# Performance work log

Hardware: AMD Instinct MI355X
Metric: run time of the kernel (lower is better)

## Reference

```python
import jax, jax.numpy as jnp
import numpy as np

B, L, DIN, H, E, K = 64, 256, 768, 64, 8, 2
S = 16  # sqrt(L): token<->feature grid side
LOSS_COEF = 1e-2


def gelu(x):
    return jax.nn.gelu(x, approximate=False)  # torch nn.GELU (exact erf)


def cv_squared(v):
    v = v.astype(jnp.float32)
    return jnp.var(v, ddof=1) / (jnp.mean(v) ** 2 + 1e-10)


def setup_inputs() -> dict:
    key = jax.random.key(0)
    ks = jax.random.split(key, 16)
    rn = lambda k, shape, s=0.02: jax.random.normal(k, shape, jnp.float32) * s
    lap = jnp.array([[0., 1., 0.], [1., -4., 1.], [0., 1., 0.]], jnp.float32)
    return {
        "x": jax.random.normal(ks[0], (B, L, DIN), jnp.float32),
        "dte": jax.random.normal(ks[1], (B, L, DIN), jnp.float32),
        "w_gate": rn(ks[2], (L, E), 1.0),
        "W_exp": rn(ks[3], (E, DIN, H)), "b_exp": jnp.zeros((E, H), jnp.float32),
        "W_sh": rn(ks[4], (DIN, H)), "b_sh": jnp.zeros((H,), jnp.float32),
        "ln_g": jnp.ones((H,), jnp.float32), "ln_b": jnp.zeros((H,), jnp.float32),
        "W_px": rn(ks[5], (H, 2 * H)), "b_px": jnp.zeros((2 * H,), jnp.float32),
        "conv_sh": jnp.tile(lap[None, None], (H, 1, 1, 1)),  # depthwise Laplacian [H,1,3,3]
        "W_pxx": rn(ks[6], (H, H)), "b_pxx": jnp.zeros((H,), jnp.float32),
        "W_dte": rn(ks[7], (H, H)), "b_dte": jnp.zeros((H,), jnp.float32),
        "W_dteall": rn(ks[8], (H, H)), "b_dteall": jnp.zeros((H,), jnp.float32),
        "W_rgb": rn(ks[9], (DIN, H)), "b_rgb": jnp.zeros((H,), jnp.float32),
        "W_fx": rn(ks[10], (H, H)), "b_fx": jnp.zeros((H,), jnp.float32),
        "W_fmod": rn(ks[11], (H, H)), "b_fmod": jnp.zeros((H,), jnp.float32),
        "W_fxx": rn(ks[12], (H, H)), "b_fxx": jnp.zeros((H,), jnp.float32),
    }


def reference(x, dte, w_gate, W_exp, b_exp, W_sh, b_sh, ln_g, ln_b, W_px, b_px,
              conv_sh, W_pxx, b_pxx, W_dte, b_dte, W_dteall, b_dteall,
              W_rgb, b_rgb, W_fx, b_fx, W_fmod, b_fmod, W_fxx, b_fxx):
    # ---- top-k gating (clean logits; noisy_gating=False / eval) ----
    logits = dte.mean(-1) @ w_gate                     # [B,E]
    topv, topi = jax.lax.top_k(logits, K)
    topg = jax.nn.softmax(topv, axis=1)
    gates = jnp.zeros_like(logits).at[jnp.arange(B)[:, None], topi].set(topg)
    importance = gates.sum(0)
    load = (gates > 0).sum(0).astype(jnp.float32)
    loss = LOSS_COEF * (cv_squared(importance) + cv_squared(load))
    # ---- sparse dispatch / expert Linear / weighted combine (dense-equivalent) ----
    y = jnp.einsum('be,bld,edh->blh', gates, dte, W_exp) + (gates @ b_exp)[:, None, :]
    # ---- shared expert Linear + Shared block ----
    sh = dte @ W_sh + b_sh                             # [B,L,H]
    shortcut = sh
    t = (sh - sh.mean(-1, keepdims=True)) * jax.lax.rsqrt(sh.var(-1, keepdims=True) + 1e-6)
    t = t * ln_g + ln_b
    t = t @ W_px + b_px                                # [B,L,2H]
    t1, t2 = t[..., :H], t[..., H:]
    f = t1.transpose(0, 2, 1).reshape(B, H, S, S)      # token2feature
    f = jax.lax.conv_general_dilated(f, conv_sh, (1, 1), 'SAME', feature_group_count=H)
    t1 = f.reshape(B, H, L).transpose(0, 2, 1)         # feature2token
    sh = (gelu(t1) * t2) @ W_pxx + b_pxx + shortcut
    # ---- combine MoE and shared streams ----
    dte_tok = (y @ W_dte + b_dte) + (sh @ W_dteall + b_dteall)
    rgb_tok = x @ W_rgb + b_rgb
    # ---- Fusion (its self.norm was overwritten to GELU; token<->feature round-trip is identity) ----
    shortcut = rgb_tok
    a = gelu(rgb_tok) @ W_fx + b_fx
    m = gelu(dte_tok) @ W_fmod + b_fmod
    out = (gelu(m) * a) @ W_fxx + b_fxx + shortcut     # [B,L,H]
    return out, loss
```

## Files before the change

### kernel.cpp

```cpp
#include <hip/hip_runtime.h>
#include <math.h>

typedef unsigned short u16;
typedef unsigned int u32;
typedef __attribute__((ext_vector_type(8))) short bf16x8;
typedef __attribute__((ext_vector_type(4))) float f32x4;


__device__ __forceinline__ float bf2f(u16 u) {
    union { u32 i; float f; } x; x.i = ((u32)u) << 16; return x.f;
}
__device__ __forceinline__ u16 f2bf(float f) {
    union { float f; u32 i; } x; x.f = f;
    u32 i = x.i;
    return (u16)((i + 0x7fffu + ((i >> 16) & 1u)) >> 16);
}
__device__ __forceinline__ u32 pack2(float a, float b) {
    return (u32)f2bf(a) | ((u32)f2bf(b) << 16);
}
__device__ __forceinline__ float wsum(float v) {
    #pragma unroll
    for (int o = 1; o < 64; o <<= 1) v += __shfl_xor(v, o, 64);
    return v;
}
__device__ __forceinline__ float gelu_f(float x) {
    return 0.5f * x * (1.0f + erff(x * 0.70710678118654752440f));
}

__global__ __launch_bounds__(256) void k_gate_part(const float* __restrict__ dte,
                                                   const float* __restrict__ w_gate,
                                                   float* __restrict__ partial) {
    __shared__ float dmeanS[64];
    int p = blockIdx.x, tid = threadIdx.x, w = tid >> 6, lane = tid & 63;
    for (int i = 0; i < 16; i++) {
        int l = w * 16 + i;
        const float* pr = dte + ((size_t)p * 64 + l) * 768;
        float s = 0.f;
        #pragma unroll
        for (int j = 0; j < 3; j++) {
            float4 v = *(const float4*)(pr + (lane + j * 64) * 4);
            s += v.x + v.y + v.z + v.w;
        }
        s = wsum(s);
        if (lane == 0) dmeanS[l] = s * (1.f / 768.f);
    }
    __syncthreads();
    if (w == 0) {
        float dm = dmeanS[lane];
        int wl = (p & 3) * 64 + lane;
        #pragma unroll
        for (int e = 0; e < 8; e++) {
            float s = wsum(dm * w_gate[wl * 8 + e]);
            if (lane == 0) partial[p * 8 + e] = s;
        }
    }
}

__global__ __launch_bounds__(256) void k_gate_fin(const float* __restrict__ partial,
                                                  const float* __restrict__ b_exp,
                                                  int* __restrict__ topi,
                                                  float* __restrict__ topg,
                                                  float* __restrict__ bias_y,
                                                  float* __restrict__ loss_out) {
    __shared__ float gS[64 * 8];
    __shared__ int i0S[64], i1S[64];
    __shared__ float g0S[64], g1S[64];
    int tid = threadIdx.x;
    if (tid < 64) {
        float lg[8];
        #pragma unroll
        for (int e = 0; e < 8; e++)
            lg[e] = partial[(tid * 4 + 0) * 8 + e] + partial[(tid * 4 + 1) * 8 + e] +
                    partial[(tid * 4 + 2) * 8 + e] + partial[(tid * 4 + 3) * 8 + e];
        int i0 = 0; float v0 = lg[0];
        #pragma unroll
        for (int e = 1; e < 8; e++) if (lg[e] > v0) { v0 = lg[e]; i0 = e; }
        int i1 = -1; float v1 = -1e30f;
        #pragma unroll
        for (int e = 0; e < 8; e++) if (e != i0 && lg[e] > v1) { v1 = lg[e]; i1 = e; }
        if (i1 < 0) i1 = (i0 + 1) & 7;
        float e2 = expf(v1 - v0);
        float g0 = 1.f / (1.f + e2);
        float g1 = e2 / (1.f + e2);
        #pragma unroll
        for (int e = 0; e < 8; e++) gS[tid * 8 + e] = 0.f;
        gS[tid * 8 + i0] = g0;
        gS[tid * 8 + i1] = g1;
        i0S[tid] = i0; i1S[tid] = i1; g0S[tid] = g0; g1S[tid] = g1;
        topi[tid * 2] = i0; topi[tid * 2 + 1] = i1;
        topg[tid * 2] = g0; topg[tid * 2 + 1] = g1;
    }
    __syncthreads();
    for (int idx = tid; idx < 4096; idx += 256) {
        int b = idx >> 6, h = idx & 63;
        bias_y[idx] = g0S[b] * b_exp[i0S[b] * 64 + h] + g1S[b] * b_exp[i1S[b] * 64 + h];
    }
    if (tid < 64) {
        float g[8];
        #pragma unroll
        for (int e = 0; e < 8; e++) g[e] = gS[tid * 8 + e];
        float imp[8], ld[8];
        #pragma unroll
        for (int e = 0; e < 8; e++) {
            imp[e] = wsum(g[e]);
            ld[e]  = wsum(g[e] > 0.f ? 1.f : 0.f);
        }
        if (tid == 0) {
            float l = 0.f;
            {
                float s = 0.f;
                #pragma unroll
                for (int e = 0; e < 8; e++) s += imp[e];
                float mn = s / 8.f, v = 0.f;
                #pragma unroll
                for (int e = 0; e < 8; e++) { float d = imp[e] - mn; v += d * d; }
                l += (v / 7.f) / (mn * mn + 1e-10f);
            }
            {
                float s = 0.f;
                #pragma unroll
                for (int e = 0; e < 8; e++) s += ld[e];
                float mn = s / 8.f, v = 0.f;
                #pragma unroll
                for (int e = 0; e < 8; e++) { float d = ld[e] - mn; v += d * d; }
                l += (v / 7.f) / (mn * mn + 1e-10f);
            }
            loss_out[0] = 0.01f * l;
        }
    }
}

__global__ __launch_bounds__(256) void k_gemm3(const float* __restrict__ dte,
                                               const float* __restrict__ x,
                                               const float* __restrict__ W_sh,
                                               const float* __restrict__ b_sh,
                                               const float* __restrict__ W_exp,
                                               const int* __restrict__ topi,
                                               const float* __restrict__ topg,
                                               const float* __restrict__ bias_y,
                                               const float* __restrict__ W_rgb,
                                               const float* __restrict__ b_rgb,
                                               float* __restrict__ buf_sh,
                                               u16* __restrict__ buf_y,
                                               float* __restrict__ out_rgb) {
    __shared__ u16 As[64 * 72];
    __shared__ u16 Wt[64 * 72];
    int bid = blockIdx.x;
    int kind, row0;
    if (bid < 512) { kind = bid & 1; row0 = (bid >> 1) * 64; }
    else           { kind = 2;       row0 = (bid - 512) * 64; }
    int b = row0 >> 8;
    int tid = threadIdx.x, wv = tid >> 6, lane = tid & 63;
    int m = lane & 15, quad = lane >> 4;

    const float* A = (kind == 2) ? x : dte;
    const float* W0 = (kind == 2) ? W_rgb : W_sh;
    const float* W1 = W0;
    float g0 = 0.f, g1 = 0.f;
    if (kind == 1) {
        W0 = W_exp + (size_t)topi[2 * b] * 49152;
        W1 = W_exp + (size_t)topi[2 * b + 1] * 49152;
        g0 = topg[2 * b]; g1 = topg[2 * b + 1];
    }

    float4 pa[2][2];
    float  pw[16];
    const int a_r  = tid >> 3;
    const int a_k8 = (tid & 7) * 8;
    const int w_n  = tid & 63;
    const int w_k0 = (tid >> 6) * 16;

    auto loadA = [&](int kc) {
        #pragma unroll
        for (int j = 0; j < 2; j++) {
            const float* src = A + (size_t)(row0 + a_r + j * 32) * 768 + kc * 64 + a_k8;
            pa[j][0] = *(const float4*)(src);
            pa[j][1] = *(const float4*)(src + 4);
        }
    };
    auto loadW = [&](int kc) {
        if (kind == 1) {
            #pragma unroll
            for (int j = 0; j < 16; j++) {
                size_t off = (size_t)(kc * 64 + w_k0 + j) * 64 + w_n;
                pw[j] = g0 * W0[off] + g1 * W1[off];
            }
        } else {
            #pragma unroll
            for (int j = 0; j < 16; j++)
                pw[j] = W0[(size_t)(kc * 64 + w_k0 + j) * 64 + w_n];
        }
    };
    auto stageLDS = [&]() {
        #pragma unroll
        for (int j = 0; j < 2; j++) {
            uint4 d;
            d.x = pack2(pa[j][0].x, pa[j][0].y);
            d.y = pack2(pa[j][0].z, pa[j][0].w);
            d.z = pack2(pa[j][1].x, pa[j][1].y);
            d.w = pack2(pa[j][1].z, pa[j][1].w);
            *(uint4*)&As[(a_r + j * 32) * 72 + a_k8] = d;
        }
        uint4 d0, d1;
        d0.x = pack2(pw[0],  pw[1]);  d0.y = pack2(pw[2],  pw[3]);
        d0.z = pack2(pw[4],  pw[5]);  d0.w = pack2(pw[6],  pw[7]);
        d1.x = pack2(pw[8],  pw[9]);  d1.y = pack2(pw[10], pw[11]);
        d1.z = pack2(pw[12], pw[13]); d1.w = pack2(pw[14], pw[15]);
        *(uint4*)&Wt[w_n * 72 + w_k0]     = d0;
        *(uint4*)&Wt[w_n * 72 + w_k0 + 8] = d1;
    };

    f32x4 acc0 = {0.f, 0.f, 0.f, 0.f}, acc1 = acc0, acc2 = acc0, acc3 = acc0;

    loadA(0); loadW(0);
    for (int kc = 0; kc < 12; kc++) {
        __syncthreads();
        stageLDS();
        __syncthreads();
        if (kc < 11) { loadA(kc + 1); loadW(kc + 1); }
        const int ar = (wv * 16 + m) * 72;
        bf16x8 a0 = *(const bf16x8*)&As[ar + quad * 8];
        bf16x8 a1 = *(const bf16x8*)&As[ar + 32 + quad * 8];
        #pragma unroll
        for (int t = 0; t < 4; t++) {
            const int br = (t * 16 + m) * 72;
            bf16x8 b0 = *(const bf16x8*)&Wt[br + quad * 8];
            bf16x8 b1 = *(const bf16x8*)&Wt[br + 32 + quad * 8];
            f32x4* accp = (t == 0) ? &acc0 : (t == 1) ? &acc1 : (t == 2) ? &acc2 : &acc3;
            *accp = __builtin_amdgcn_mfma_f32_16x16x32_bf16(a0, b0, *accp, 0, 0, 0);
            *accp = __builtin_amdgcn_mfma_f32_16x16x32_bf16(a1, b1, *accp, 0, 0, 0);
        }
    }

    f32x4 accs[4] = {acc0, acc1, acc2, acc3};
    #pragma unroll
    for (int t = 0; t < 4; t++) {
        int col = t * 16 + m;
        float bias;
        if (kind == 0)      bias = b_sh[col];
        else if (kind == 1) bias = bias_y[b * 64 + col];
        else                bias = b_rgb[col];
        #pragma unroll
        for (int i = 0; i < 4; i++) {
            int r = row0 + wv * 16 + quad * 4 + i;
            float val = accs[t][i] + bias;
            if (kind == 0)      buf_sh[(size_t)r * 64 + col] = val;
            else if (kind == 1) buf_y[(size_t)r * 64 + col] = f2bf(val);
            else                out_rgb[(size_t)r * 64 + col] = val;
        }
    }
}

__global__ __launch_bounds__(256) void k_lnpx(const float* __restrict__ buf_sh,
                                              const float* __restrict__ ln_g,
                                              const float* __restrict__ ln_b,
                                              const float* __restrict__ W_px,
                                              const float* __restrict__ b_px,
                                              u16* __restrict__ t1, u16* __restrict__ t2) {
    __shared__ float T[16 * 68];
    __shared__ float Wpx[8192];
    int r0 = blockIdx.x * 16;
    int tid = threadIdx.x, w = tid >> 6, lane = tid & 63;
    #pragma unroll
    for (int j = 0; j < 8; j++) {
        int e4 = tid + j * 256;
        *(float4*)(Wpx + e4 * 4) = *(const float4*)(W_px + e4 * 4);
    }
    float lnG = ln_g[lane], lnB = ln_b[lane];
    #pragma unroll
    for (int i = 0; i < 4; i++) {
        int l = w * 4 + i;
        float v = buf_sh[(size_t)(r0 + l) * 64 + lane];
        float mean = wsum(v) * (1.f / 64.f);
        float d = v - mean;
        float var = wsum(d * d) * (1.f / 64.f);
        T[l * 68 + lane] = d * rsqrtf(var + 1e-6f) * lnG + lnB;
    }
    __syncthreads();
    int rg = tid >> 4, cg = tid & 15;
    float acc1[4] = {}, acc2[4] = {};
    const float* tr = T + rg * 68;
    #pragma unroll 4
    for (int kk = 0; kk < 64; kk++) {
        float a0 = tr[kk];
        float4 w1 = *(const float4*)(Wpx + kk * 128 + cg * 4);
        float4 w2 = *(const float4*)(Wpx + kk * 128 + 64 + cg * 4);
        acc1[0] += a0 * w1.x; acc1[1] += a0 * w1.y; acc1[2] += a0 * w1.z; acc1[3] += a0 * w1.w;
        acc2[0] += a0 * w2.x; acc2[1] += a0 * w2.y; acc2[2] += a0 * w2.z; acc2[3] += a0 * w2.w;
    }
    float4 b1 = *(const float4*)(b_px + cg * 4);
    float4 b2 = *(const float4*)(b_px + 64 + cg * 4);
    {
        int r = r0 + rg;
        u32* d1 = (u32*)(t1 + (size_t)r * 64 + cg * 4);
        d1[0] = pack2(acc1[0] + b1.x, acc1[1] + b1.y);
        d1[1] = pack2(acc1[2] + b1.z, acc1[3] + b1.w);
        u32* d2 = (u32*)(t2 + (size_t)r * 64 + cg * 4);
        d2[0] = pack2(acc2[0] + b2.x, acc2[1] + b2.y);
        d2[1] = pack2(acc2[2] + b2.z, acc2[3] + b2.w);
    }
}

__global__ __launch_bounds__(256) void k_tail(const u16* __restrict__ t1,
                                              const u16* __restrict__ t2,
                                              const float* __restrict__ conv_sh,
                                              const float* __restrict__ W_pxx,
                                              const float* __restrict__ b_pxx,
                                              const float* __restrict__ buf_sh,
                                              const u16* __restrict__ buf_y,
                                              const float* __restrict__ W_dte,
                                              const float* __restrict__ b_dte,
                                              const float* __restrict__ W_dteall,
                                              const float* __restrict__ b_dteall,
                                              const float* __restrict__ W_fx,
                                              const float* __restrict__ b_fx,
                                              const float* __restrict__ W_fmod,
                                              const float* __restrict__ b_fmod,
                                              const float* __restrict__ W_fxx,
                                              const float* __restrict__ b_fxx,
                                              float* __restrict__ out) {
    __shared__ float C0[16 * 68];
    __shared__ float Yb[16 * 68];
    __shared__ float GA[16 * 68];
    __shared__ float SH1[16 * 68];
    __shared__ float GM[16 * 68];
    __shared__ float RS[16 * 64];
    int r0 = blockIdx.x * 16;
    int tid = threadIdx.x, w = tid >> 6, lane = tid & 63;
    int rg = tid >> 4, cg = tid & 15;

    {
        int l = tid >> 4, c = (tid & 15) * 4;
        uint2 v = *(const uint2*)(buf_y + (size_t)(r0 + l) * 64 + c);
        Yb[l * 68 + c + 0] = bf2f((u16)(v.x & 0xffffu));
        Yb[l * 68 + c + 1] = bf2f((u16)(v.x >> 16));
        Yb[l * 68 + c + 2] = bf2f((u16)(v.y & 0xffffu));
        Yb[l * 68 + c + 3] = bf2f((u16)(v.y >> 16));
    }
    {
        int l = tid >> 4, c4 = tid & 15;
        float4 rv = *(const float4*)(out + (size_t)(r0 + l) * 64 + c4 * 4);
        *(float4*)(RS + l * 64 + c4 * 4) = rv;
        GA[l * 68 + c4 * 4 + 0] = gelu_f(rv.x);
        GA[l * 68 + c4 * 4 + 1] = gelu_f(rv.y);
        GA[l * 68 + c4 * 4 + 2] = gelu_f(rv.z);
        GA[l * 68 + c4 * 4 + 3] = gelu_f(rv.w);
    }
    {
        float c0 = conv_sh[lane * 9 + 0], c1 = conv_sh[lane * 9 + 1], c2 = conv_sh[lane * 9 + 2];
        float c3 = conv_sh[lane * 9 + 3], c4 = conv_sh[lane * 9 + 4], c5 = conv_sh[lane * 9 + 5];
        float c6 = conv_sh[lane * 9 + 6], c7 = conv_sh[lane * 9 + 7], c8 = conv_sh[lane * 9 + 8];
        #pragma unroll
        for (int i = 0; i < 4; i++) {
            int l = w * 4 + i;
            int gr = r0 + l;
            int pix = gr & 255, ii = pix >> 4, jj = pix & 15;
            const u16* p = t1 + (size_t)gr * 64 + lane;
            float c = c4 * bf2f(p[0]);
            if (ii > 0) {
                c += c1 * bf2f(p[-1024]);
                if (jj > 0)  c += c0 * bf2f(p[-1024 - 64]);
                if (jj < 15) c += c2 * bf2f(p[-1024 + 64]);
            }
            if (jj > 0)  c += c3 * bf2f(p[-64]);
            if (jj < 15) c += c5 * bf2f(p[64]);
            if (ii < 15) {
                c += c7 * bf2f(p[1024]);
                if (jj > 0)  c += c6 * bf2f(p[1024 - 64]);
                if (jj < 15) c += c8 * bf2f(p[1024 + 64]);
            }
            C0[l * 68 + lane] = gelu_f(c) * bf2f(t2[(size_t)gr * 64 + lane]);
        }
    }
    __syncthreads();

    {
        float acc[4] = {};
        const float* ur = C0 + rg * 68;
        #pragma unroll 8
        for (int kk = 0; kk < 64; kk++) {
            float a0 = ur[kk];
            float4 wvv = *(const float4*)(W_pxx + kk * 64 + cg * 4);
            acc[0] += a0 * wvv.x; acc[1] += a0 * wvv.y; acc[2] += a0 * wvv.z; acc[3] += a0 * wvv.w;
        }
        float4 bp = *(const float4*)(b_pxx + cg * 4);
        float4 shv = *(const float4*)(buf_sh + (size_t)(r0 + rg) * 64 + cg * 4);
        *(float4*)(SH1 + rg * 68 + cg * 4) =
            make_float4(acc[0] + bp.x + shv.x, acc[1] + bp.y + shv.y,
                        acc[2] + bp.z + shv.z, acc[3] + bp.w + shv.w);
    }
    __syncthreads();

    {
        float acc[4] = {};
        const float* yr = Yb + rg * 68;
        const float* sr = SH1 + rg * 68;
        #pragma unroll 4
        for (int kk = 0; kk < 64; kk++) {
            float y0 = yr[kk];
            float s0 = sr[kk];
            float4 w1 = *(const float4*)(W_dte + kk * 64 + cg * 4);
            float4 w2 = *(const float4*)(W_dteall + kk * 64 + cg * 4);
            acc[0] += y0 * w1.x + s0 * w2.x; acc[1] += y0 * w1.y + s0 * w2.y;
            acc[2] += y0 * w1.z + s0 * w2.z; acc[3] += y0 * w1.w + s0 * w2.w;
        }
        float4 bd1 = *(const float4*)(b_dte + cg * 4);
        float4 bd2 = *(const float4*)(b_dteall + cg * 4);
        *(float4*)(GM + rg * 68 + cg * 4) =
            make_float4(gelu_f(acc[0] + bd1.x + bd2.x), gelu_f(acc[1] + bd1.y + bd2.y),
                        gelu_f(acc[2] + bd1.z + bd2.z), gelu_f(acc[3] + bd1.w + bd2.w));
    }
    __syncthreads();

    {
        float accA[4] = {}, accM[4] = {};
        const float* ga = GA + rg * 68;
        const float* gm = GM + rg * 68;
        #pragma unroll 4
        for (int kk = 0; kk < 64; kk++) {
            float a0 = ga[kk];
            float m0 = gm[kk];
            float4 wa = *(const float4*)(W_fx + kk * 64 + cg * 4);
            float4 wm = *(const float4*)(W_fmod + kk * 64 + cg * 4);
            accA[0] += a0 * wa.x; accA[1] += a0 * wa.y; accA[2] += a0 * wa.z; accA[3] += a0 * wa.w;
            accM[0] += m0 * wm.x; accM[1] += m0 * wm.y; accM[2] += m0 * wm.z; accM[3] += m0 * wm.w;
        }
        float4 bx = *(const float4*)(b_fx + cg * 4);
        float4 bm = *(const float4*)(b_fmod + cg * 4);
        float a0 = accA[0] + bx.x, a1 = accA[1] + bx.y, a2 = accA[2] + bx.z, a3 = accA[3] + bx.w;
        float m0 = accM[0] + bm.x, m1 = accM[1] + bm.y, m2 = accM[2] + bm.z, m3 = accM[3] + bm.w;
        *(float4*)(C0 + rg * 68 + cg * 4) =
            make_float4(gelu_f(m0) * a0, gelu_f(m1) * a1, gelu_f(m2) * a2, gelu_f(m3) * a3);
    }
    __syncthreads();

    {
        float acc[4] = {};
        const float* pr = C0 + rg * 68;
        #pragma unroll 8
        for (int kk = 0; kk < 64; kk++) {
            float p0 = pr[kk];
            float4 wvv = *(const float4*)(W_fxx + kk * 64 + cg * 4);
            acc[0] += p0 * wvv.x; acc[1] += p0 * wvv.y; acc[2] += p0 * wvv.z; acc[3] += p0 * wvv.w;
        }
        float4 bo = *(const float4*)(b_fxx + cg * 4);
        *(float4*)(out + (size_t)(r0 + rg) * 64 + cg * 4) =
            make_float4(acc[0] + bo.x + RS[rg * 64 + cg * 4 + 0],
                        acc[1] + bo.y + RS[rg * 64 + cg * 4 + 1],
                        acc[2] + bo.z + RS[rg * 64 + cg * 4 + 2],
                        acc[3] + bo.w + RS[rg * 64 + cg * 4 + 3]);
    }
}

extern "C" void kernel_launch(void* const* d_in, const int* in_sizes, int n_in,
                              void* d_out, int out_size, void* d_ws, size_t ws_size,
                              hipStream_t stream) {
    const float* x       = (const float*)d_in[0];
    const float* dte     = (const float*)d_in[1];
    const float* w_gate  = (const float*)d_in[2];
    const float* W_exp   = (const float*)d_in[3];
    const float* b_exp   = (const float*)d_in[4];
    const float* W_sh    = (const float*)d_in[5];
    const float* b_sh    = (const float*)d_in[6];
    const float* ln_g    = (const float*)d_in[7];
    const float* ln_b    = (const float*)d_in[8];
    const float* W_px    = (const float*)d_in[9];
    const float* b_px    = (const float*)d_in[10];
    const float* conv_sh = (const float*)d_in[11];
    const float* W_pxx   = (const float*)d_in[12];
    const float* b_pxx   = (const float*)d_in[13];
    const float* W_dte   = (const float*)d_in[14];
    const float* b_dte   = (const float*)d_in[15];
    const float* W_dteall= (const float*)d_in[16];
    const float* b_dteall= (const float*)d_in[17];
    const float* W_rgb   = (const float*)d_in[18];
    const float* b_rgb   = (const float*)d_in[19];
    const float* W_fx    = (const float*)d_in[20];
    const float* b_fx    = (const float*)d_in[21];
    const float* W_fmod  = (const float*)d_in[22];
    const float* b_fmod  = (const float*)d_in[23];
    const float* W_fxx   = (const float*)d_in[24];
    const float* b_fxx   = (const float*)d_in[25];

    float* out = (float*)d_out;

    float* wsf    = (float*)d_ws;
    float* partial= wsf;
    int*   topi   = (int*)(wsf + 2048);
    float* topg   = wsf + 2176;
    float* bias_y = wsf + 2304;
    float* buf_sh = wsf + 8192;
    u16*   buf_y  = (u16*)(wsf + 8192 + 1048576);
    u16*   t1     = (u16*)(wsf + 8192 + 1048576 + 524288);
    u16*   t2     = (u16*)(wsf + 8192 + 1048576 + 524288*2);

    hipLaunchKernelGGL(k_gate_part, dim3(256), dim3(256), 0, stream, dte, w_gate, partial);
    hipLaunchKernelGGL(k_gate_fin, dim3(1), dim3(256), 0, stream,
                       partial, b_exp, topi, topg, bias_y, out + 1048576);
    hipLaunchKernelGGL(k_gemm3, dim3(768), dim3(256), 0, stream,
                       dte, x, W_sh, b_sh, W_exp, topi, topg, bias_y, W_rgb, b_rgb,
                       buf_sh, buf_y, out);
    hipLaunchKernelGGL(k_lnpx, dim3(1024), dim3(256), 0, stream,
                       buf_sh, ln_g, ln_b, W_px, b_px, t1, t2);
    hipLaunchKernelGGL(k_tail, dim3(1024), dim3(256), 0, stream,
                       t1, t2, conv_sh, W_pxx, b_pxx, buf_sh, buf_y,
                       W_dte, b_dte, W_dteall, b_dteall,
                       W_fx, b_fx, W_fmod, b_fmod, W_fxx, b_fxx, out);

    (void)in_sizes; (void)n_in; (void)out_size; (void)ws_size;
}
```

Baseline: 267.4 us.

## Stage tail weights through double-buffered LDS and double rows per lnpx block

Measured after the change: 258.6 us. 3.3% less time.

```diff
diff --git a/kernel.cpp b/kernel.cpp
--- a/kernel.cpp
+++ b/kernel.cpp
@@ -257,9 +257,9 @@
                                               const float* __restrict__ W_px,
                                               const float* __restrict__ b_px,
                                               u16* __restrict__ t1, u16* __restrict__ t2) {
-    __shared__ float T[16 * 68];
+    __shared__ float T[32 * 68];
     __shared__ float Wpx[8192];
-    int r0 = blockIdx.x * 16;
+    int r0 = blockIdx.x * 32;
     int tid = threadIdx.x, w = tid >> 6, lane = tid & 63;
     #pragma unroll
     for (int j = 0; j < 8; j++) {
@@ -267,9 +267,8 @@
         *(float4*)(Wpx + e4 * 4) = *(const float4*)(W_px + e4 * 4);
     }
     float lnG = ln_g[lane], lnB = ln_b[lane];
-    #pragma unroll
-    for (int i = 0; i < 4; i++) {
-        int l = w * 4 + i;
+    for (int i = 0; i < 8; i++) {
+        int l = w * 8 + i;
         float v = buf_sh[(size_t)(r0 + l) * 64 + lane];
         float mean = wsum(v) * (1.f / 64.f);
         float d = v - mean;
@@ -278,26 +277,29 @@
     }
     __syncthreads();
     int rg = tid >> 4, cg = tid & 15;
-    float acc1[4] = {}, acc2[4] = {};
-    const float* tr = T + rg * 68;
+    float acc1[2][4] = {}, acc2[2][4] = {};
+    const float* tr = T + rg * 2 * 68;
     #pragma unroll 4
     for (int kk = 0; kk < 64; kk++) {
-        float a0 = tr[kk];
+        float a0 = tr[kk], a1 = tr[68 + kk];
         float4 w1 = *(const float4*)(Wpx + kk * 128 + cg * 4);
         float4 w2 = *(const float4*)(Wpx + kk * 128 + 64 + cg * 4);
-        acc1[0] += a0 * w1.x; acc1[1] += a0 * w1.y; acc1[2] += a0 * w1.z; acc1[3] += a0 * w1.w;
-        acc2[0] += a0 * w2.x; acc2[1] += a0 * w2.y; acc2[2] += a0 * w2.z; acc2[3] += a0 * w2.w;
+        acc1[0][0] += a0 * w1.x; acc1[0][1] += a0 * w1.y; acc1[0][2] += a0 * w1.z; acc1[0][3] += a0 * w1.w;
+        acc1[1][0] += a1 * w1.x; acc1[1][1] += a1 * w1.y; acc1[1][2] += a1 * w1.z; acc1[1][3] += a1 * w1.w;
+        acc2[0][0] += a0 * w2.x; acc2[0][1] += a0 * w2.y; acc2[0][2] += a0 * w2.z; acc2[0][3] += a0 * w2.w;
+        acc2[1][0] += a1 * w2.x; acc2[1][1] += a1 * w2.y; acc2[1][2] += a1 * w2.z; acc2[1][3] += a1 * w2.w;
     }
     float4 b1 = *(const float4*)(b_px + cg * 4);
     float4 b2 = *(const float4*)(b_px + 64 + cg * 4);
-    {
-        int r = r0 + rg;
+    #pragma unroll
+    for (int i = 0; i < 2; i++) {
+        int r = r0 + rg * 2 + i;
         u32* d1 = (u32*)(t1 + (size_t)r * 64 + cg * 4);
-        d1[0] = pack2(acc1[0] + b1.x, acc1[1] + b1.y);
-        d1[1] = pack2(acc1[2] + b1.z, acc1[3] + b1.w);
+        d1[0] = pack2(acc1[i][0] + b1.x, acc1[i][1] + b1.y);
+        d1[1] = pack2(acc1[i][2] + b1.z, acc1[i][3] + b1.w);
         u32* d2 = (u32*)(t2 + (size_t)r * 64 + cg * 4);
-        d2[0] = pack2(acc2[0] + b2.x, acc2[1] + b2.y);
-        d2[1] = pack2(acc2[2] + b2.z, acc2[3] + b2.w);
+        d2[0] = pack2(acc2[i][0] + b2.x, acc2[i][1] + b2.y);
+        d2[1] = pack2(acc2[i][2] + b2.z, acc2[i][3] + b2.w);
     }
 }
 
@@ -320,31 +322,39 @@
                                               const float* __restrict__ b_fxx,
                                               float* __restrict__ out) {
     __shared__ float C0[16 * 68];
-    __shared__ float Yb[16 * 68];
     __shared__ float GA[16 * 68];
     __shared__ float SH1[16 * 68];
     __shared__ float GM[16 * 68];
-    __shared__ float RS[16 * 64];
+    __shared__ u16   Ybh[16 * 72];
+    __shared__ float WL[2][4096];
     int r0 = blockIdx.x * 16;
     int tid = threadIdx.x, w = tid >> 6, lane = tid & 63;
     int rg = tid >> 4, cg = tid & 15;
 
-    {
-        int l = tid >> 4, c = (tid & 15) * 4;
-        uint2 v = *(const uint2*)(buf_y + (size_t)(r0 + l) * 64 + c);
-        Yb[l * 68 + c + 0] = bf2f((u16)(v.x & 0xffffu));
-        Yb[l * 68 + c + 1] = bf2f((u16)(v.x >> 16));
-        Yb[l * 68 + c + 2] = bf2f((u16)(v.y & 0xffffu));
-        Yb[l * 68 + c + 3] = bf2f((u16)(v.y >> 16));
-    }
-    {
-        int l = tid >> 4, c4 = tid & 15;
-        float4 rv = *(const float4*)(out + (size_t)(r0 + l) * 64 + c4 * 4);
-        *(float4*)(RS + l * 64 + c4 * 4) = rv;
-        GA[l * 68 + c4 * 4 + 0] = gelu_f(rv.x);
-        GA[l * 68 + c4 * 4 + 1] = gelu_f(rv.y);
-        GA[l * 68 + c4 * 4 + 2] = gelu_f(rv.z);
-        GA[l * 68 + c4 * 4 + 3] = gelu_f(rv.w);
+    float4 wbuf[4];
+    auto wload = [&](const float* Wsrc) {
+        #pragma unroll
+        for (int j = 0; j < 4; j++)
+            wbuf[j] = *(const float4*)(Wsrc + (tid + j * 256) * 4);
+    };
+    auto wstore = [&](int half) {
+        #pragma unroll
+        for (int j = 0; j < 4; j++)
+            *(float4*)(&WL[half][(tid + j * 256) * 4]) = wbuf[j];
+    };
+
+    wload(W_pxx);
+    float4 rsv;
+    {
+        uint2 v = *(const uint2*)(buf_y + (size_t)(r0 + rg) * 64 + cg * 4);
+        *(uint2*)(&Ybh[rg * 72 + cg * 4]) = v;
+    }
+    {
+        rsv = *(const float4*)(out + (size_t)(r0 + rg) * 64 + cg * 4);
+        GA[rg * 68 + cg * 4 + 0] = gelu_f(rsv.x);
+        GA[rg * 68 + cg * 4 + 1] = gelu_f(rsv.y);
+        GA[rg * 68 + cg * 4 + 2] = gelu_f(rsv.z);
+        GA[rg * 68 + cg * 4 + 3] = gelu_f(rsv.w);
     }
     {
         float c0 = conv_sh[lane * 9 + 0], c1 = conv_sh[lane * 9 + 1], c2 = conv_sh[lane * 9 + 2];
@@ -372,16 +382,18 @@
             C0[l * 68 + lane] = gelu_f(c) * bf2f(t2[(size_t)gr * 64 + lane]);
         }
     }
-    __syncthreads();
-
+    wstore(0);
+    __syncthreads();
+
+    wload(W_dte);
     {
         float acc[4] = {};
         const float* ur = C0 + rg * 68;
         #pragma unroll 8
         for (int kk = 0; kk < 64; kk++) {
             float a0 = ur[kk];
-            float4 wvv = *(const float4*)(W_pxx + kk * 64 + cg * 4);
-            acc[0] += a0 * wvv.x; acc[1] += a0 * wvv.y; acc[2] += a0 * wvv.z; acc[3] += a0 * wvv.w;
+            float4 wv = *(const float4*)(&WL[0][kk * 64 + cg * 4]);
+            acc[0] += a0 * wv.x; acc[1] += a0 * wv.y; acc[2] += a0 * wv.z; acc[3] += a0 * wv.w;
         }
         float4 bp = *(const float4*)(b_pxx + cg * 4);
         float4 shv = *(const float4*)(buf_sh + (size_t)(r0 + rg) * 64 + cg * 4);
@@ -389,41 +401,64 @@
             make_float4(acc[0] + bp.x + shv.x, acc[1] + bp.y + shv.y,
                         acc[2] + bp.z + shv.z, acc[3] + bp.w + shv.w);
     }
-    __syncthreads();
-
-    {
-        float acc[4] = {};
-        const float* yr = Yb + rg * 68;
+    wstore(1);
+    __syncthreads();
+
+    float accC[4] = {};
+    wload(W_dteall);
+    {
+        const u16* yr = Ybh + rg * 72;
+        #pragma unroll 8
+        for (int kk = 0; kk < 64; kk++) {
+            float y0 = bf2f(yr[kk]);
+            float4 wv = *(const float4*)(&WL[1][kk * 64 + cg * 4]);
+            accC[0] += y0 * wv.x; accC[1] += y0 * wv.y; accC[2] += y0 * wv.z; accC[3] += y0 * wv.w;
+        }
+    }
+    wstore(0);
+    __syncthreads();
+
+    wload(W_fx);
+    {
         const float* sr = SH1 + rg * 68;
-        #pragma unroll 4
+        #pragma unroll 8
         for (int kk = 0; kk < 64; kk++) {
-            float y0 = yr[kk];
             float s0 = sr[kk];
-            float4 w1 = *(const float4*)(W_dte + kk * 64 + cg * 4);
-            float4 w2 = *(const float4*)(W_dteall + kk * 64 + cg * 4);
-            acc[0] += y0 * w1.x + s0 * w2.x; acc[1] += y0 * w1.y + s0 * w2.y;
-            acc[2] += y0 * w1.z + s0 * w2.z; acc[3] += y0 * w1.w + s0 * w2.w;
+            float4 wv = *(const float4*)(&WL[0][kk * 64 + cg * 4]);
+            accC[0] += s0 * wv.x; accC[1] += s0 * wv.y; accC[2] += s0 * wv.z; accC[3] += s0 * wv.w;
         }
         float4 bd1 = *(const float4*)(b_dte + cg * 4);
         float4 bd2 = *(const float4*)(b_dteall + cg * 4);
         *(float4*)(GM + rg * 68 + cg * 4) =
-            make_float4(gelu_f(acc[0] + bd1.x + bd2.x), gelu_f(acc[1] + bd1.y + bd2.y),
-                        gelu_f(acc[2] + bd1.z + bd2.z), gelu_f(acc[3] + bd1.w + bd2.w));
-    }
-    __syncthreads();
-
-    {
-        float accA[4] = {}, accM[4] = {};
+            make_float4(gelu_f(accC[0] + bd1.x + bd2.x), gelu_f(accC[1] + bd1.y + bd2.y),
+                        gelu_f(accC[2] + bd1.z + bd2.z), gelu_f(accC[3] + bd1.w + bd2.w));
+    }
+    wstore(1);
+    __syncthreads();
+
+    float accA[4] = {};
+    wload(W_fmod);
+    {
         const float* ga = GA + rg * 68;
-        const float* gm = GM + rg * 68;
-        #pragma unroll 4
+        #pragma unroll 8
         for (int kk = 0; kk < 64; kk++) {
             float a0 = ga[kk];
+            float4 wv = *(const float4*)(&WL[1][kk * 64 + cg * 4]);
+            accA[0] += a0 * wv.x; accA[1] += a0 * wv.y; accA[2] += a0 * wv.z; accA[3] += a0 * wv.w;
+        }
+    }
+    wstore(0);
+    __syncthreads();
+
+    wload(W_fxx);
+    {
+        float accM[4] = {};
+        const float* gm = GM + rg * 68;
+        #pragma unroll 8
+        for (int kk = 0; kk < 64; kk++) {
             float m0 = gm[kk];
-            float4 wa = *(const float4*)(W_fx + kk * 64 + cg * 4);
-            float4 wm = *(const float4*)(W_fmod + kk * 64 + cg * 4);
-            accA[0] += a0 * wa.x; accA[1] += a0 * wa.y; accA[2] += a0 * wa.z; accA[3] += a0 * wa.w;
-            accM[0] += m0 * wm.x; accM[1] += m0 * wm.y; accM[2] += m0 * wm.z; accM[3] += m0 * wm.w;
+            float4 wv = *(const float4*)(&WL[0][kk * 64 + cg * 4]);
+            accM[0] += m0 * wv.x; accM[1] += m0 * wv.y; accM[2] += m0 * wv.z; accM[3] += m0 * wv.w;
         }
         float4 bx = *(const float4*)(b_fx + cg * 4);
         float4 bm = *(const float4*)(b_fmod + cg * 4);
@@ -432,6 +467,7 @@
         *(float4*)(C0 + rg * 68 + cg * 4) =
             make_float4(gelu_f(m0) * a0, gelu_f(m1) * a1, gelu_f(m2) * a2, gelu_f(m3) * a3);
     }
+    wstore(1);
     __syncthreads();
 
     {
@@ -440,15 +476,13 @@
         #pragma unroll 8
         for (int kk = 0; kk < 64; kk++) {
             float p0 = pr[kk];
-            float4 wvv = *(const float4*)(W_fxx + kk * 64 + cg * 4);
-            acc[0] += p0 * wvv.x; acc[1] += p0 * wvv.y; acc[2] += p0 * wvv.z; acc[3] += p0 * wvv.w;
+            float4 wv = *(const float4*)(&WL[1][kk * 64 + cg * 4]);
+            acc[0] += p0 * wv.x; acc[1] += p0 * wv.y; acc[2] += p0 * wv.z; acc[3] += p0 * wv.w;
         }
         float4 bo = *(const float4*)(b_fxx + cg * 4);
         *(float4*)(out + (size_t)(r0 + rg) * 64 + cg * 4) =
-            make_float4(acc[0] + bo.x + RS[rg * 64 + cg * 4 + 0],
-                        acc[1] + bo.y + RS[rg * 64 + cg * 4 + 1],
-                        acc[2] + bo.z + RS[rg * 64 + cg * 4 + 2],
-                        acc[3] + bo.w + RS[rg * 64 + cg * 4 + 3]);
+            make_float4(acc[0] + bo.x + rsv.x, acc[1] + bo.y + rsv.y,
+                        acc[2] + bo.z + rsv.z, acc[3] + bo.w + rsv.w);
     }
 }
 
@@ -500,7 +534,7 @@
     hipLaunchKernelGGL(k_gemm3, dim3(768), dim3(256), 0, stream,
                        dte, x, W_sh, b_sh, W_exp, topi, topg, bias_y, W_rgb, b_rgb,
                        buf_sh, buf_y, out);
-    hipLaunchKernelGGL(k_lnpx, dim3(1024), dim3(256), 0, stream,
+    hipLaunchKernelGGL(k_lnpx, dim3(512), dim3(256), 0, stream,
                        buf_sh, ln_g, ln_b, W_px, b_px, t1, t2);
     hipLaunchKernelGGL(k_tail, dim3(1024), dim3(256), 0, stream,
                        t1, t2, conv_sh, W_pxx, b_pxx, buf_sh, buf_y,
```
